# Optimization experiments

Hardware: AMD Instinct MI355X
Metric: run time of the kernel (lower is better)

## Reference

```python
import jax, jax.numpy as jnp
import numpy as np

C = 512
GROUPS = 8
EPS = 1e-5


def setup_inputs() -> dict:
    key = jax.random.key(0)
    ks = jax.random.split(key, 7)
    B, H, W = 16, 32, 32
    x = jax.random.normal(ks[0], (B, C, H, W), dtype=jnp.float32)
    gamma = jnp.ones((C,), jnp.float32)
    beta = jnp.zeros((C,), jnp.float32)
    # 1x1 convs stored as [out, in] matrices
    w_qkv = jax.random.normal(ks[1], (3 * C, C), dtype=jnp.float32) * (1.0 / np.sqrt(C))
    b_qkv = jax.random.normal(ks[2], (3 * C,), dtype=jnp.float32) * 0.02
    w_proj = jax.random.normal(ks[3], (C, C), dtype=jnp.float32) * (1.0 / np.sqrt(C))
    b_proj = jax.random.normal(ks[4], (C,), dtype=jnp.float32) * 0.02
    return {"x": x, "gamma": gamma, "beta": beta, "w_qkv": w_qkv,
            "b_qkv": b_qkv, "w_proj": w_proj, "b_proj": b_proj}


def _group_norm(x, gamma, beta):
    B, Cc, H, W = x.shape
    xg = x.reshape(B, GROUPS, Cc // GROUPS, H, W)
    mean = xg.mean(axis=(2, 3, 4), keepdims=True)
    var = xg.var(axis=(2, 3, 4), keepdims=True)
    xg = (xg - mean) * jax.lax.rsqrt(var + EPS)
    x = xg.reshape(B, Cc, H, W)
    return x * gamma[None, :, None, None] + beta[None, :, None, None]


def reference(x, gamma, beta, w_qkv, b_qkv, w_proj, b_proj):
    B, Cc, H, W = x.shape
    N = H * W
    h = _group_norm(x, gamma, beta)  # [B,C,H,W]
    hf = h.reshape(B, Cc, N)  # [B,C,N]
    # 1x1 conv == matmul over channel dim
    qkv = jnp.einsum('oc,bcn->bon', w_qkv, hf) + b_qkv[None, :, None]  # [B,3C,N]
    q, k, v = jnp.split(qkv, 3, axis=1)  # each [B,C,N]
    scale = 1.0 / jnp.sqrt(jnp.float32(Cc))
    # attn[b,i,j] = sum_c q[b,c,i] * k[b,c,j]
    attn = jnp.einsum('bci,bcj->bij', q, k) * scale  # [B,N,N]
    attn = jax.nn.softmax(attn, axis=-1)
    out = jnp.einsum('bij,bcj->bci', attn, v)  # [B,C,N]
    out = jnp.einsum('oc,bcn->bon', w_proj, out) + b_proj[None, :, None]
    return x + out.reshape(B, Cc, H, W)
```

## Files before the change

### kernel.cpp

```cpp
#include <hip/hip_runtime.h>
#include <hip/hip_bf16.h>

typedef unsigned short u16;
typedef unsigned int u32;
typedef __attribute__((ext_vector_type(8))) short short8;
typedef __attribute__((ext_vector_type(4))) float floatx4;

#define BATCH 16
#define CDIM 512
#define NSPAT 1024
#define NGROUP 8

__device__ __forceinline__ u16 f2bf(float f) {
    unsigned u = __float_as_uint(f);
    u += 0x7FFFu + ((u >> 16) & 1u);
    return (u16)(u >> 16);
}
__device__ __forceinline__ u32 f2bf2(float lo, float hi) {
    __hip_bfloat162 h = __float22bfloat162_rn(make_float2(lo, hi));
    return *(u32*)&h;
}

__device__ __forceinline__ void load_lds16(const void* g, void* l) {
    __builtin_amdgcn_global_load_lds(
        (const __attribute__((address_space(1))) unsigned int*)g,
        (__attribute__((address_space(3))) unsigned int*)l, 16, 0, 0);
}

#define SBAR0 __builtin_amdgcn_sched_barrier(0)
#define BARRIER { SBAR0; __builtin_amdgcn_s_barrier(); SBAR0; }

__global__ __launch_bounds__(256) void prep_kernel(
    const float* __restrict__ w_qkv, const float* __restrict__ w_proj,
    const float* __restrict__ b_qkv, const float* __restrict__ x,
    u16* __restrict__ wmega, u16* __restrict__ wproj_bf, u16* __restrict__ wv_t,
    float* __restrict__ stats, float* __restrict__ lsums, float* __restrict__ bpv) {
    int b = blockIdx.x;
    int tid = threadIdx.x;
    if (b < 768) {
        const float* src = (b < 512) ? w_qkv : w_proj;
        u16* dst = (b < 512) ? wmega : wproj_bf;
        int i = (b < 512 ? b : b - 512) * 256 + tid;
        float4 v = ((const float4*)src)[i];
        u32* d = (u32*)dst;
        d[i * 2] = f2bf2(v.x, v.y);
        d[i * 2 + 1] = f2bf2(v.z, v.w);
        return;
    }
    if (b < 832) {
        __shared__ u16 t[64 * 66];
        int bt = b - 768;
        int tx = bt & 7, ty = bt >> 3;
        const float* src = w_qkv + (size_t)(1024 + ty * 64) * CDIM + tx * 64;
#pragma unroll
        for (int p = 0; p < 4; ++p) {
            int r = p * 16 + (tid >> 4);
            int c4 = (tid & 15) << 2;
            float4 v = *(const float4*)(src + (size_t)r * CDIM + c4);
            u16* d = &t[r * 66 + c4];
            d[0] = f2bf(v.x); d[1] = f2bf(v.y); d[2] = f2bf(v.z); d[3] = f2bf(v.w);
        }
        __syncthreads();
        u16* dst = wv_t + (size_t)(tx * 64) * CDIM + ty * 64;
#pragma unroll
        for (int p = 0; p < 4; ++p) {
            int c = p * 16 + (tid >> 4);
            int r4 = (tid & 15) << 2;
            ushort4 o;
            o.x = t[(r4 + 0) * 66 + c];
            o.y = t[(r4 + 1) * 66 + c];
            o.z = t[(r4 + 2) * 66 + c];
            o.w = t[(r4 + 3) * 66 + c];
            *(ushort4*)(dst + (size_t)c * CDIM + r4) = o;
        }
        return;
    }
    if (b < 960) {
        __shared__ float rs[4], rss[4];
        int bg = b - 832;
        const float4* xv = (const float4*)(x + (size_t)bg * 65536);
        float s = 0.f, ss = 0.f;
        for (int i = tid; i < 16384; i += 256) {
            float4 v = xv[i];
            s += v.x + v.y + v.z + v.w;
            ss += v.x * v.x + v.y * v.y + v.z * v.z + v.w * v.w;
        }
#pragma unroll
        for (int off = 32; off; off >>= 1) { s += __shfl_down(s, off); ss += __shfl_down(ss, off); }
        int wave = tid >> 6, lane = tid & 63;
        if (lane == 0) { rs[wave] = s; rss[wave] = ss; }
        __syncthreads();
        if (tid == 0) {
            float S1 = rs[0] + rs[1] + rs[2] + rs[3];
            float S2 = rss[0] + rss[1] + rss[2] + rss[3];
            float mean = S1 * (1.f / 65536.f);
            float var = S2 * (1.f / 65536.f) - mean * mean;
            stats[bg * 2] = mean;
            stats[bg * 2 + 1] = rsqrtf(var + 1e-5f);
        }
        return;
    }
    if (b < 976) {
        ((float4*)lsums)[(b - 960) * 256 + tid] = (float4){0.f, 0.f, 0.f, 0.f};
        return;
    }
    {
        int o0 = (b - 976) * 64;
        int wave = tid >> 6, lane = tid & 63;
        const float4* bvv = (const float4*)(b_qkv + 1024);
        float4 v0 = bvv[lane * 2], v1 = bvv[lane * 2 + 1];
        for (int it = 0; it < 16; ++it) {
            int o = o0 + wave * 16 + it;
            const float4* wr = (const float4*)(w_proj + (size_t)o * CDIM);
            float4 a0 = wr[lane * 2], a1 = wr[lane * 2 + 1];
            float s = a0.x * v0.x + a0.y * v0.y + a0.z * v0.z + a0.w * v0.w
                    + a1.x * v1.x + a1.y * v1.y + a1.z * v1.z + a1.w * v1.w;
#pragma unroll
            for (int off = 32; off; off >>= 1) s += __shfl_down(s, off);
            if (lane == 0) bpv[o] = s;
        }
    }
}

__device__ __forceinline__ void stage_tile(
    const u16* __restrict__ Ab, const u16* __restrict__ Bb, int lda, int ldb,
    int m0, int n0, int k0, u16* As, u16* Bs) {
    int tid = threadIdx.x;
#pragma unroll
    for (int it = 0; it < 4; ++it) {
        int c = it * 256 + tid;
        int r = c >> 3, p = c & 7;
        int kc = p ^ (r & 7);
        load_lds16(Ab + (size_t)(m0 + r) * lda + k0 + (kc << 3), &As[c << 3]);
        load_lds16(Bb + (size_t)(n0 + r) * ldb + k0 + (kc << 3), &Bs[c << 3]);
    }
}

__device__ __forceinline__ void compute_tile(
    const u16* As, const u16* Bs, int wm, int wn, int quad, int lrow,
    floatx4 (&acc)[4][4]) {
#pragma unroll
    for (int s = 0; s < 2; ++s) {
        short8 af[4], bf[4];
#pragma unroll
        for (int i = 0; i < 4; ++i) {
            int R = wm + i * 16 + lrow;
            int p = (s * 4 + quad) ^ (R & 7);
            af[i] = *(const short8*)&As[(R << 6) + (p << 3)];
        }
#pragma unroll
        for (int j = 0; j < 4; ++j) {
            int R = wn + j * 16 + lrow;
            int p = (s * 4 + quad) ^ (R & 7);
            bf[j] = *(const short8*)&Bs[(R << 6) + (p << 3)];
        }
#pragma unroll
        for (int i = 0; i < 4; ++i)
#pragma unroll
            for (int j = 0; j < 4; ++j)
                acc[i][j] = __builtin_amdgcn_mfma_f32_16x16x32_bf16(af[i], bf[j], acc[i][j], 0, 0, 0);
    }
}

__device__ __forceinline__ void gemm_core_sb(
    const u16* __restrict__ Ab, const u16* __restrict__ Bb, int K, int lda, int ldb,
    int m0, int n0, u16* As, u16* Bs, floatx4 (&acc)[4][4]) {
    int tid = threadIdx.x;
    int lane = tid & 63, wave = tid >> 6, quad = lane >> 4, lrow = lane & 15;
    int wm = (wave >> 1) << 6, wn = (wave & 1) << 6;
    for (int k0 = 0; k0 < K; k0 += 64) {
        stage_tile(Ab, Bb, lda, ldb, m0, n0, k0, As, Bs);
        __syncthreads();
        compute_tile(As, Bs, wm, wn, quad, lrow, acc);
        __syncthreads();
    }
}

#define ACC_INIT floatx4 acc[4][4]; \
    _Pragma("unroll") for (int i = 0; i < 4; ++i) \
    _Pragma("unroll") for (int j = 0; j < 4; ++j) acc[i][j] = (floatx4){0.f, 0.f, 0.f, 0.f};

#define EPILOG_IDX int lane = threadIdx.x & 63, wave = threadIdx.x >> 6; \
    int quad = lane >> 4, lrow = lane & 15; \
    int wm = (wave >> 1) << 6, wn = (wave & 1) << 6;

__device__ __forceinline__ void issueA2(
    const u16* __restrict__ Ab, int lda, int m0, int t, int h, u16* smem) {
    int tid = threadIdx.x;
    u16* base = smem + (t & 1) * 16384 + h * 8192;
#pragma unroll
    for (int l = 0; l < 2; ++l) {
        int c = l * 512 + tid;
        int rho = c >> 3, p = c & 7;
        int kc = p ^ (rho & 7);
        int r = ((rho >> 6) << 7) | (h << 6) | (rho & 63);
        load_lds16(Ab + (size_t)(m0 + r) * lda + (t << 6) + (kc << 3), base + (c << 3));
    }
}
__device__ __forceinline__ void issueB2(
    const u16* __restrict__ Bb, int ldb, int n0, int t, int h, u16* smem) {
    int tid = threadIdx.x;
    u16* base = smem + 32768 + (t & 1) * 16384 + h * 8192;
#pragma unroll
    for (int l = 0; l < 2; ++l) {
        int c = l * 512 + tid;
        int rho = c >> 3, p = c & 7;
        int kc = p ^ (rho & 7);
        int r = ((rho >> 5) << 6) | (h << 5) | (rho & 31);
        load_lds16(Bb + (size_t)(n0 + r) * ldb + (t << 6) + (kc << 3), base + (c << 3));
    }
}

template <bool RD_AF, int QM, int QN>
__device__ __forceinline__ void comp2(
    const u16* smem, int slot, int wrow, int wcol, int quad, int lrow,
    short8 (&af)[8], floatx4 (&acc)[8][4]) {
    const u16* Ah = smem + slot * 16384 + QM * 8192;
    const u16* Bh = smem + 32768 + slot * 16384 + QN * 8192;
    short8 bf[4];
#pragma unroll
    for (int ks = 0; ks < 2; ++ks) {
        if (RD_AF) {
#pragma unroll
            for (int i = 0; i < 4; ++i) {
                int rho = wrow * 64 + i * 16 + lrow;
                int p = (ks * 4 + quad) ^ (lrow & 7);
                af[ks * 4 + i] = *(const short8*)&Ah[(rho << 6) + (p << 3)];
            }
        }
#pragma unroll
        for (int j = 0; j < 2; ++j) {
            int rho = wcol * 32 + j * 16 + lrow;
            int p = (ks * 4 + quad) ^ (lrow & 7);
            bf[ks * 2 + j] = *(const short8*)&Bh[(rho << 6) + (p << 3)];
        }
    }
    asm volatile("s_waitcnt lgkmcnt(0)" ::: "memory");
    SBAR0;
    __builtin_amdgcn_s_setprio(1);
#pragma unroll
    for (int ks = 0; ks < 2; ++ks)
#pragma unroll
        for (int i = 0; i < 4; ++i)
#pragma unroll
            for (int j = 0; j < 2; ++j)
                acc[QM * 4 + i][QN * 2 + j] = __builtin_amdgcn_mfma_f32_16x16x32_bf16(
                    af[ks * 4 + i], bf[ks * 2 + j], acc[QM * 4 + i][QN * 2 + j], 0, 0, 0);
    __builtin_amdgcn_s_setprio(0);
}

__device__ __forceinline__ void gemm256x256(
    const u16* __restrict__ Ab, const u16* __restrict__ Bb, int K, int lda, int ldb,
    int m0, int n0, u16* smem, floatx4 (&acc)[8][4]) {
    int tid = threadIdx.x;
    int lane = tid & 63, wave = tid >> 6;
    int quad = lane >> 4, lrow = lane & 15;
    int wrow = wave >> 2, wcol = wave & 3;
    int nt = K >> 6;
    short8 af[8];
    issueA2(Ab, lda, m0, 0, 0, smem);
    issueB2(Bb, ldb, n0, 0, 0, smem);
    issueB2(Bb, ldb, n0, 0, 1, smem);
    issueA2(Ab, lda, m0, 0, 1, smem);
    for (int t = 0; t < nt; ++t) {
        int slot = t & 1;
        bool nxt = (t + 1 < nt);
        asm volatile("s_waitcnt vmcnt(4)" ::: "memory");
        BARRIER;
        if (nxt) issueA2(Ab, lda, m0, t + 1, 0, smem);
        comp2<true, 0, 0>(smem, slot, wrow, wcol, quad, lrow, af, acc);
        BARRIER;
        if (nxt) { asm volatile("s_waitcnt vmcnt(4)" ::: "memory"); }
        else     { asm volatile("s_waitcnt vmcnt(2)" ::: "memory"); }
        BARRIER;
        if (nxt) issueB2(Bb, ldb, n0, t + 1, 0, smem);
        comp2<false, 0, 1>(smem, slot, wrow, wcol, quad, lrow, af, acc);
        BARRIER;
        if (nxt) { asm volatile("s_waitcnt vmcnt(4)" ::: "memory"); }
        else     { asm volatile("s_waitcnt vmcnt(0)" ::: "memory"); }
        BARRIER;
        if (nxt) issueB2(Bb, ldb, n0, t + 1, 1, smem);
        comp2<true, 1, 0>(smem, slot, wrow, wcol, quad, lrow, af, acc);
        BARRIER;
        if (nxt) issueA2(Ab, lda, m0, t + 1, 1, smem);
        comp2<false, 1, 1>(smem, slot, wrow, wcol, quad, lrow, af, acc);
        BARRIER;
    }
}

__device__ __forceinline__ void issueA4(
    const u16* __restrict__ Ab, int lda, int m0, int t, u16* smem) {
    int tid = threadIdx.x;
    u16* base = smem + (t & 1) * 16384;
#pragma unroll
    for (int l = 0; l < 4; ++l) {
        int c = l * 512 + tid;
        int rho = c >> 3, p = c & 7;
        int kc = p ^ (rho & 7);
        load_lds16(Ab + (size_t)(m0 + rho) * lda + (t << 6) + (kc << 3), base + (c << 3));
    }
}
__device__ __forceinline__ void issueB4(
    const u16* __restrict__ Bb, int ldb, int n0, int t, int h, u16* smem) {
    int tid = threadIdx.x;
    u16* base = smem + 32768 + (t & 1) * 8192 + h * 4096;
    int rho = tid >> 3, p = tid & 7;
    int kc = p ^ (rho & 7);
    int r = ((rho >> 5) << 6) | (h << 5) | (rho & 31);
    load_lds16(Bb + (size_t)(n0 + r) * ldb + (t << 6) + (kc << 3), base + (tid << 3));
}

template <bool RD_AF, int QN>
__device__ __forceinline__ void comp4(
    const u16* smem, int slot, int wrow, int wcol, int quad, int lrow,
    short8 (&af)[8], floatx4 (&acc)[4][4]) {
    const u16* Ah = smem + slot * 16384;
    const u16* Bh = smem + 32768 + slot * 8192 + QN * 4096;
    short8 bf[4];
#pragma unroll
    for (int ks = 0; ks < 2; ++ks) {
        if (RD_AF) {
#pragma unroll
            for (int i = 0; i < 4; ++i) {
                int rho = wrow * 64 + i * 16 + lrow;
                int p = (ks * 4 + quad) ^ (lrow & 7);
                af[ks * 4 + i] = *(const short8*)&Ah[(rho << 6) + (p << 3)];
            }
        }
#pragma unroll
        for (int j = 0; j < 2; ++j) {
            int rho = wcol * 32 + j * 16 + lrow;
            int p = (ks * 4 + quad) ^ (lrow & 7);
            bf[ks * 2 + j] = *(const short8*)&Bh[(rho << 6) + (p << 3)];
        }
    }
    asm volatile("s_waitcnt lgkmcnt(0)" ::: "memory");
    SBAR0;
    __builtin_amdgcn_s_setprio(1);
#pragma unroll
    for (int ks = 0; ks < 2; ++ks)
#pragma unroll
        for (int i = 0; i < 4; ++i)
#pragma unroll
            for (int j = 0; j < 2; ++j)
                acc[i][QN * 2 + j] = __builtin_amdgcn_mfma_f32_16x16x32_bf16(
                    af[ks * 4 + i], bf[ks * 2 + j], acc[i][QN * 2 + j], 0, 0, 0);
    __builtin_amdgcn_s_setprio(0);
}

__device__ __forceinline__ void gemm256x128(
    const u16* __restrict__ Ab, const u16* __restrict__ Bb, int K, int lda, int ldb,
    int m0, int n0, u16* smem, floatx4 (&acc)[4][4]) {
    int tid = threadIdx.x;
    int lane = tid & 63, wave = tid >> 6;
    int quad = lane >> 4, lrow = lane & 15;
    int wrow = wave >> 1, wcol = wave & 1;
    int nt = K >> 6;
    short8 af[8];
    issueB4(Bb, ldb, n0, 0, 0, smem);
    issueA4(Ab, lda, m0, 0, smem);
    issueB4(Bb, ldb, n0, 0, 1, smem);
    for (int t = 0; t < nt; ++t) {
        int slot = t & 1;
        bool nxt = (t + 1 < nt);
        asm volatile("s_waitcnt vmcnt(1)" ::: "memory");
        BARRIER;
        if (nxt) { issueB4(Bb, ldb, n0, t + 1, 0, smem); issueA4(Ab, lda, m0, t + 1, smem); }
        comp4<true, 0>(smem, slot, wrow, wcol, quad, lrow, af, acc);
        BARRIER;
        if (nxt) { asm volatile("s_waitcnt vmcnt(5)" ::: "memory"); }
        else     { asm volatile("s_waitcnt vmcnt(0)" ::: "memory"); }
        BARRIER;
        if (nxt) issueB4(Bb, ldb, n0, t + 1, 1, smem);
        comp4<false, 1>(smem, slot, wrow, wcol, quad, lrow, af, acc);
        BARRIER;
    }
}

#define ACC_INIT84 floatx4 acc[8][4]; \
    _Pragma("unroll") for (int i = 0; i < 8; ++i) \
    _Pragma("unroll") for (int j = 0; j < 4; ++j) acc[i][j] = (floatx4){0.f, 0.f, 0.f, 0.f};

#define ACC_INIT44 floatx4 acc[4][4]; \
    _Pragma("unroll") for (int i = 0; i < 4; ++i) \
    _Pragma("unroll") for (int j = 0; j < 4; ++j) acc[i][j] = (floatx4){0.f, 0.f, 0.f, 0.f};

#define TSTR 66
__global__ __launch_bounds__(256) void gn_wpv_kernel(
    const float* __restrict__ x, const float* __restrict__ gamma, const float* __restrict__ beta,
    const float* __restrict__ stats, u16* __restrict__ hT,
    const u16* __restrict__ wproj_bf, const u16* __restrict__ wv_t, u16* __restrict__ wmega) {
    __shared__ u16 smem[2 * 128 * 64];
    int tid = threadIdx.x;
    if (blockIdx.z == 16) {
        if (blockIdx.x >= 4 || blockIdx.y >= 4) return;
        int m0 = blockIdx.y << 7, n0 = blockIdx.x << 7;
        ACC_INIT;
        gemm_core_sb(wproj_bf, wv_t, CDIM, CDIM, CDIM, m0, n0, smem, smem + 128 * 64, acc);
        EPILOG_IDX;
#pragma unroll
        for (int i = 0; i < 4; ++i)
#pragma unroll
            for (int j = 0; j < 4; ++j)
#pragma unroll
                for (int r = 0; r < 4; ++r) {
                    int R = m0 + wm + i * 16 + (quad << 2) + r;
                    int Cc = n0 + wn + j * 16 + lrow;
                    wmega[(size_t)(1024 + R) * CDIM + Cc] = f2bf(acc[i][j][r]);
                }
        return;
    }
    u16* t = smem;
    int b = blockIdx.z, c0 = blockIdx.y << 6, n0 = blockIdx.x << 6;
    const float* xb = x + ((size_t)b * CDIM + c0) * NSPAT + n0;
#pragma unroll
    for (int p = 0; p < 4; ++p) {
        int cl = p * 16 + (tid >> 4);
        int nl = (tid & 15) << 2;
        int c = c0 + cl;
        int bg = b * NGROUP + (c >> 6);
        float ga = gamma[c] * stats[bg * 2 + 1];
        float be = beta[c] - stats[bg * 2] * ga;
        float4 v = *(const float4*)(xb + (size_t)cl * NSPAT + nl);
        u16* dst = &t[cl * TSTR + nl];
        dst[0] = f2bf(v.x * ga + be);
        dst[1] = f2bf(v.y * ga + be);
        dst[2] = f2bf(v.z * ga + be);
        dst[3] = f2bf(v.w * ga + be);
    }
    __syncthreads();
    u16* hb = hT + ((size_t)b * NSPAT + n0) * CDIM + c0;
#pragma unroll
    for (int p = 0; p < 4; ++p) {
        int nl = p * 16 + (tid >> 4);
        int cl4 = (tid & 15) << 2;
        ushort4 o;
        o.x = t[(cl4 + 0) * TSTR + nl];
        o.y = t[(cl4 + 1) * TSTR + nl];
        o.z = t[(cl4 + 2) * TSTR + nl];
        o.w = t[(cl4 + 3) * TSTR + nl];
        *(ushort4*)(hb + (size_t)nl * CDIM + cl4) = o;
    }
}

__global__ __launch_bounds__(512, 2) void qkv_kernel(
    const u16* __restrict__ wmega, const u16* __restrict__ hT,
    const float* __restrict__ b_qkv, const float* __restrict__ bpv,
    u16* __restrict__ qkT, u16* __restrict__ WV) {
    extern __shared__ u16 smem[];
    int z = blockIdx.x;
    int n0 = blockIdx.y << 8;
    int m0 = blockIdx.z << 8;
    const u16* Bb = hT + (size_t)z * CDIM * NSPAT;
    ACC_INIT84;
    gemm256x256(wmega, Bb, CDIM, CDIM, CDIM, m0, n0, smem, acc);
    int lane = threadIdx.x & 63, wave = threadIdx.x >> 6;
    int quad = lane >> 4, lrow = lane & 15;
    int wrow = wave >> 2, wcol = wave & 3;
    if (blockIdx.z < 4) {
        u16* qk = qkT + (size_t)z * NSPAT * NSPAT;
#pragma unroll
        for (int mf = 0; mf < 8; ++mf) {
            int R0 = m0 + wrow * 128 + mf * 16 + (quad << 2);
            float4 bv = *(const float4*)&b_qkv[R0];
#pragma unroll
            for (int nf = 0; nf < 4; ++nf) {
                int Cc = n0 + wcol * 64 + nf * 16 + lrow;
                uint2 u;
                u.x = f2bf2(acc[mf][nf][0] + bv.x, acc[mf][nf][1] + bv.y);
                u.y = f2bf2(acc[mf][nf][2] + bv.z, acc[mf][nf][3] + bv.w);
                *(uint2*)&qk[(size_t)Cc * NSPAT + R0] = u;
            }
        }
    } else {
        u16* Wp = WV + (size_t)z * CDIM * NSPAT;
#pragma unroll
        for (int mf = 0; mf < 8; ++mf) {
            int R = m0 - 1024 + wrow * 128 + mf * 16 + (quad << 2);
            float4 pv = *(const float4*)&bpv[R];
#pragma unroll
            for (int nf = 0; nf < 4; ++nf) {
                int Cc = n0 + wcol * 64 + nf * 16 + lrow;
                Wp[(size_t)(R + 0) * NSPAT + Cc] = f2bf(acc[mf][nf][0] + pv.x);
                Wp[(size_t)(R + 1) * NSPAT + Cc] = f2bf(acc[mf][nf][1] + pv.y);
                Wp[(size_t)(R + 2) * NSPAT + Cc] = f2bf(acc[mf][nf][2] + pv.z);
                Wp[(size_t)(R + 3) * NSPAT + Cc] = f2bf(acc[mf][nf][3] + pv.w);
            }
        }
    }
}

__global__ __launch_bounds__(512, 2) void scores_kernel(
    const u16* __restrict__ qkT, u16* __restrict__ P, float* __restrict__ lsums, float scale) {
    extern __shared__ u16 smem[];
    int z = blockIdx.x;
    int n0 = blockIdx.y << 8;
    int m0 = blockIdx.z << 8;
    const u16* qb = qkT + (size_t)z * NSPAT * NSPAT;
    ACC_INIT84;
    gemm256x256(qb + CDIM, qb, CDIM, NSPAT, NSPAT, m0, n0, smem, acc);
    int lane = threadIdx.x & 63, wave = threadIdx.x >> 6;
    int quad = lane >> 4, lrow = lane & 15;
    int wrow = wave >> 2, wcol = wave & 3;
    u16* Pp = P + (size_t)z * NSPAT * NSPAT;
    float* ls = lsums + (size_t)z * NSPAT;
#pragma unroll
    for (int nf = 0; nf < 4; ++nf) {
        int Ci = n0 + wcol * 64 + nf * 16 + lrow;
        float part = 0.f;
#pragma unroll
        for (int mf = 0; mf < 8; ++mf) {
            int Rj0 = m0 + wrow * 128 + mf * 16 + (quad << 2);
            float e0 = __expf(acc[mf][nf][0] * scale);
            float e1 = __expf(acc[mf][nf][1] * scale);
            float e2 = __expf(acc[mf][nf][2] * scale);
            float e3 = __expf(acc[mf][nf][3] * scale);
            part += (e0 + e1) + (e2 + e3);
            uint2 u;
            u.x = f2bf2(e0, e1);
            u.y = f2bf2(e2, e3);
            *(uint2*)&Pp[(size_t)Ci * NSPAT + Rj0] = u;
        }
        part += __shfl_xor(part, 16);
        part += __shfl_xor(part, 32);
        if (lane < 16) atomicAdd(&ls[Ci], part);
    }
}

__global__ __launch_bounds__(512, 2) void final_kernel(
    const u16* __restrict__ WV, const u16* __restrict__ P, const float* __restrict__ lsums,
    const float* __restrict__ bias, const float* __restrict__ x, float* __restrict__ out) {
    extern __shared__ u16 smem[];
    int z = blockIdx.x;
    int n0 = blockIdx.y << 7;
    int m0 = blockIdx.z << 8;
    const u16* Pb = P + (size_t)z * NSPAT * NSPAT;
    const u16* WVb = WV + (size_t)z * CDIM * NSPAT;
    ACC_INIT44;
    gemm256x128(Pb, WVb, NSPAT, NSPAT, NSPAT, m0, n0, smem, acc);
    int lane = threadIdx.x & 63, wave = threadIdx.x >> 6;
    int quad = lane >> 4, lrow = lane & 15;
    int wrow = wave >> 1, wcol = wave & 1;
    float* Op = out + (size_t)z * CDIM * NSPAT;
    const float* xr = x + (size_t)z * CDIM * NSPAT;
    const float* li = lsums + (size_t)z * NSPAT;
#pragma unroll
    for (int mf = 0; mf < 4; ++mf) {
        int Ri0 = m0 + wrow * 64 + mf * 16 + (quad << 2);
        float4 lv = *(const float4*)&li[Ri0];
        float s0 = __builtin_amdgcn_rcpf(lv.x);
        float s1 = __builtin_amdgcn_rcpf(lv.y);
        float s2 = __builtin_amdgcn_rcpf(lv.z);
        float s3 = __builtin_amdgcn_rcpf(lv.w);
#pragma unroll
        for (int nf = 0; nf < 4; ++nf) {
            int Co = n0 + wcol * 64 + nf * 16 + lrow;
            float bv = bias[Co];
            size_t off = (size_t)Co * NSPAT + Ri0;
            float4 xv = *(const float4*)&xr[off];
            float4 o;
            o.x = acc[mf][nf][0] * s0 + bv + xv.x;
            o.y = acc[mf][nf][1] * s1 + bv + xv.y;
            o.z = acc[mf][nf][2] * s2 + bv + xv.z;
            o.w = acc[mf][nf][3] * s3 + bv + xv.w;
            *(float4*)&Op[off] = o;
        }
    }
}

extern "C" void kernel_launch(void* const* d_in, const int* in_sizes, int n_in,
                              void* d_out, int out_size, void* d_ws, size_t ws_size,
                              hipStream_t stream) {
    const float* x      = (const float*)d_in[0];
    const float* gamma  = (const float*)d_in[1];
    const float* beta   = (const float*)d_in[2];
    const float* w_qkv  = (const float*)d_in[3];
    const float* b_qkv  = (const float*)d_in[4];
    const float* w_proj = (const float*)d_in[5];
    const float* b_proj = (const float*)d_in[6];
    float* out = (float*)d_out;

    const size_t CN = (size_t)CDIM * NSPAT;
    const size_t NN = (size_t)NSPAT * NSPAT;
    const float SCALE = 0.044194173824159216f;
    const int LDS_BIG = 131072;
    const int LDS_MED = 98304;

    static bool lds_attr_done = false;
    if (!lds_attr_done) {
        hipFuncSetAttribute((const void*)qkv_kernel,
                            hipFuncAttributeMaxDynamicSharedMemorySize, LDS_BIG);
        hipFuncSetAttribute((const void*)scores_kernel,
                            hipFuncAttributeMaxDynamicSharedMemorySize, LDS_BIG);
        hipFuncSetAttribute((const void*)final_kernel,
                            hipFuncAttributeMaxDynamicSharedMemorySize, LDS_MED);
        lds_attr_done = true;
    }

    char* ws = (char*)d_ws;
    float* stats   = (float*)ws;
    float* bpv     = (float*)(ws + 1024);
    u16* wmega     = (u16*)(ws + 4096);
    u16* wproj_bf  = wmega + (size_t)3 * CDIM * CDIM;
    u16* wv_t      = wproj_bf + (size_t)CDIM * CDIM;
    u16* hT        = wv_t + (size_t)CDIM * CDIM;
    u16* qkT       = hT + BATCH * CN;
    u16* WV        = qkT + BATCH * NN;
    u16* P         = WV + BATCH * CN;
    float* lsums   = (float*)(P + BATCH * NN);

    prep_kernel<<<984, 256, 0, stream>>>(
        w_qkv, w_proj, b_qkv, x, wmega, wproj_bf, wv_t, stats, lsums, bpv);

    gn_wpv_kernel<<<dim3(16, 8, 17), 256, 0, stream>>>(
        x, gamma, beta, stats, hT, wproj_bf, wv_t, wmega);

    qkv_kernel<<<dim3(BATCH, 4, 6), 512, LDS_BIG, stream>>>(
        wmega, hT, b_qkv, bpv, qkT, WV);

    scores_kernel<<<dim3(BATCH, 4, 4), 512, LDS_BIG, stream>>>(qkT, P, lsums, SCALE);

    final_kernel<<<dim3(BATCH, 4, 4), 512, LDS_MED, stream>>>(WV, P, lsums, b_proj, x, out);
}
```

Measured before the change: 138.7 us.

## Simplify GEMM mainloops to whole-tile prefetch with one wait per K-step

Replaces the fine-grained quarter-tile ping-pong schedules in the 256x256 and 256x128 GEMM loops. The old loops issued loads for the next tile piece by piece, with barriers and setprio around each sub-compute. The new loops prefetch the whole next K-tile at the start of each iteration, wait until the current tile has landed, then run all MFMAs in one block. This removes many barriers and waitcnts, but loads are no longer interleaved with compute at sub-tile granularity. Register pressure also rises because all B fragments are held at once.

```diff
diff --git a/kernel.cpp b/kernel.cpp
--- a/kernel.cpp
+++ b/kernel.cpp
@@ -211,169 +211,146 @@
     }
 }
 
-template <bool RD_AF, int QM, int QN>
-__device__ __forceinline__ void comp2(
-    const u16* smem, int slot, int wrow, int wcol, int quad, int lrow,
-    short8 (&af)[8], floatx4 (&acc)[8][4]) {
-    const u16* Ah = smem + slot * 16384 + QM * 8192;
-    const u16* Bh = smem + 32768 + slot * 16384 + QN * 8192;
-    short8 bf[4];
-#pragma unroll
-    for (int ks = 0; ks < 2; ++ks) {
-        if (RD_AF) {
+__device__ __forceinline__ void gemm256x256(
+    const u16* __restrict__ Ab, const u16* __restrict__ Bb, int K, int lda, int ldb,
+    int m0, int n0, u16* smem, floatx4 (&acc)[8][4]) {
+    int tid = threadIdx.x;
+    int lane = tid & 63, wave = tid >> 6;
+    int quad = lane >> 4, lrow = lane & 15;
+    int wrow = wave >> 2, wcol = wave & 3;
+    int nt = K >> 6;
+    issueA2(Ab, lda, m0, 0, 0, smem);
+    issueA2(Ab, lda, m0, 0, 1, smem);
+    issueB2(Bb, ldb, n0, 0, 0, smem);
+    issueB2(Bb, ldb, n0, 0, 1, smem);
+    for (int t = 0; t < nt; ++t) {
+        int slot = t & 1;
+        BARRIER;
+        if (t + 1 < nt) {
+            issueA2(Ab, lda, m0, t + 1, 0, smem);
+            issueA2(Ab, lda, m0, t + 1, 1, smem);
+            issueB2(Bb, ldb, n0, t + 1, 0, smem);
+            issueB2(Bb, ldb, n0, t + 1, 1, smem);
+            asm volatile("s_waitcnt vmcnt(8)" ::: "memory");
+        } else {
+            asm volatile("s_waitcnt vmcnt(0)" ::: "memory");
+        }
+        BARRIER;
+        const u16* Ah = smem + slot * 16384;
+        const u16* Bh = smem + 32768 + slot * 16384;
+        short8 bf[2][4];
+#pragma unroll
+        for (int qn = 0; qn < 2; ++qn)
+#pragma unroll
+            for (int ks = 0; ks < 2; ++ks)
+#pragma unroll
+                for (int j = 0; j < 2; ++j) {
+                    int rho = wcol * 32 + j * 16 + lrow;
+                    int p = (ks * 4 + quad) ^ (lrow & 7);
+                    bf[qn][ks * 2 + j] = *(const short8*)&Bh[qn * 8192 + (rho << 6) + (p << 3)];
+                }
+#pragma unroll
+        for (int qm = 0; qm < 2; ++qm) {
+            short8 af[8];
+#pragma unroll
+            for (int ks = 0; ks < 2; ++ks)
+#pragma unroll
+                for (int i = 0; i < 4; ++i) {
+                    int rho = wrow * 64 + i * 16 + lrow;
+                    int p = (ks * 4 + quad) ^ (lrow & 7);
+                    af[ks * 4 + i] = *(const short8*)&Ah[qm * 8192 + (rho << 6) + (p << 3)];
+                }
+#pragma unroll
+            for (int ks = 0; ks < 2; ++ks)
+#pragma unroll
+                for (int i = 0; i < 4; ++i)
+#pragma unroll
+                    for (int qn = 0; qn < 2; ++qn)
+#pragma unroll
+                        for (int j = 0; j < 2; ++j)
+                            acc[qm * 4 + i][qn * 2 + j] = __builtin_amdgcn_mfma_f32_16x16x32_bf16(
+                                af[ks * 4 + i], bf[qn][ks * 2 + j], acc[qm * 4 + i][qn * 2 + j], 0, 0, 0);
+        }
+    }
+}
+
+__device__ __forceinline__ void issueA4(
+    const u16* __restrict__ Ab, int lda, int m0, int t, u16* smem) {
+    int tid = threadIdx.x;
+    u16* base = smem + (t & 1) * 16384;
+#pragma unroll
+    for (int l = 0; l < 4; ++l) {
+        int c = l * 512 + tid;
+        int rho = c >> 3, p = c & 7;
+        int kc = p ^ (rho & 7);
+        load_lds16(Ab + (size_t)(m0 + rho) * lda + (t << 6) + (kc << 3), base + (c << 3));
+    }
+}
+__device__ __forceinline__ void issueB4(
+    const u16* __restrict__ Bb, int ldb, int n0, int t, int h, u16* smem) {
+    int tid = threadIdx.x;
+    u16* base = smem + 32768 + (t & 1) * 8192 + h * 4096;
+    int rho = tid >> 3, p = tid & 7;
+    int kc = p ^ (rho & 7);
+    int r = ((rho >> 5) << 6) | (h << 5) | (rho & 31);
+    load_lds16(Bb + (size_t)(n0 + r) * ldb + (t << 6) + (kc << 3), base + (tid << 3));
+}
+
+__device__ __forceinline__ void gemm256x128(
+    const u16* __restrict__ Ab, const u16* __restrict__ Bb, int K, int lda, int ldb,
+    int m0, int n0, u16* smem, floatx4 (&acc)[4][4]) {
+    int tid = threadIdx.x;
+    int lane = tid & 63, wave = tid >> 6;
+    int quad = lane >> 4, lrow = lane & 15;
+    int wrow = wave >> 1, wcol = wave & 1;
+    int nt = K >> 6;
+    issueA4(Ab, lda, m0, 0, smem);
+    issueB4(Bb, ldb, n0, 0, 0, smem);
+    issueB4(Bb, ldb, n0, 0, 1, smem);
+    for (int t = 0; t < nt; ++t) {
+        int slot = t & 1;
+        BARRIER;
+        if (t + 1 < nt) {
+            issueA4(Ab, lda, m0, t + 1, smem);
+            issueB4(Bb, ldb, n0, t + 1, 0, smem);
+            issueB4(Bb, ldb, n0, t + 1, 1, smem);
+            asm volatile("s_waitcnt vmcnt(6)" ::: "memory");
+        } else {
+            asm volatile("s_waitcnt vmcnt(0)" ::: "memory");
+        }
+        BARRIER;
+        const u16* Ah = smem + slot * 16384;
+        const u16* Bh = smem + 32768 + slot * 8192;
+        short8 bf[2][4];
+#pragma unroll
+        for (int qn = 0; qn < 2; ++qn)
+#pragma unroll
+            for (int ks = 0; ks < 2; ++ks)
+#pragma unroll
+                for (int j = 0; j < 2; ++j) {
+                    int rho = wcol * 32 + j * 16 + lrow;
+                    int p = (ks * 4 + quad) ^ (lrow & 7);
+                    bf[qn][ks * 2 + j] = *(const short8*)&Bh[qn * 4096 + (rho << 6) + (p << 3)];
+                }
+        short8 af[8];
+#pragma unroll
+        for (int ks = 0; ks < 2; ++ks)
 #pragma unroll
             for (int i = 0; i < 4; ++i) {
                 int rho = wrow * 64 + i * 16 + lrow;
                 int p = (ks * 4 + quad) ^ (lrow & 7);
                 af[ks * 4 + i] = *(const short8*)&Ah[(rho << 6) + (p << 3)];
             }
-        }
-#pragma unroll
-        for (int j = 0; j < 2; ++j) {
-            int rho = wcol * 32 + j * 16 + lrow;
-            int p = (ks * 4 + quad) ^ (lrow & 7);
-            bf[ks * 2 + j] = *(const short8*)&Bh[(rho << 6) + (p << 3)];
-        }
-    }
-    asm volatile("s_waitcnt lgkmcnt(0)" ::: "memory");
-    SBAR0;
-    __builtin_amdgcn_s_setprio(1);
-#pragma unroll
-    for (int ks = 0; ks < 2; ++ks)
-#pragma unroll
-        for (int i = 0; i < 4; ++i)
-#pragma unroll
-            for (int j = 0; j < 2; ++j)
-                acc[QM * 4 + i][QN * 2 + j] = __builtin_amdgcn_mfma_f32_16x16x32_bf16(
-                    af[ks * 4 + i], bf[ks * 2 + j], acc[QM * 4 + i][QN * 2 + j], 0, 0, 0);
-    __builtin_amdgcn_s_setprio(0);
-}
-
-__device__ __forceinline__ void gemm256x256(
-    const u16* __restrict__ Ab, const u16* __restrict__ Bb, int K, int lda, int ldb,
-    int m0, int n0, u16* smem, floatx4 (&acc)[8][4]) {
-    int tid = threadIdx.x;
-    int lane = tid & 63, wave = tid >> 6;
-    int quad = lane >> 4, lrow = lane & 15;
-    int wrow = wave >> 2, wcol = wave & 3;
-    int nt = K >> 6;
-    short8 af[8];
-    issueA2(Ab, lda, m0, 0, 0, smem);
-    issueB2(Bb, ldb, n0, 0, 0, smem);
-    issueB2(Bb, ldb, n0, 0, 1, smem);
-    issueA2(Ab, lda, m0, 0, 1, smem);
-    for (int t = 0; t < nt; ++t) {
-        int slot = t & 1;
-        bool nxt = (t + 1 < nt);
-        asm volatile("s_waitcnt vmcnt(4)" ::: "memory");
-        BARRIER;
-        if (nxt) issueA2(Ab, lda, m0, t + 1, 0, smem);
-        comp2<true, 0, 0>(smem, slot, wrow, wcol, quad, lrow, af, acc);
-        BARRIER;
-        if (nxt) { asm volatile("s_waitcnt vmcnt(4)" ::: "memory"); }
-        else     { asm volatile("s_waitcnt vmcnt(2)" ::: "memory"); }
-        BARRIER;
-        if (nxt) issueB2(Bb, ldb, n0, t + 1, 0, smem);
-        comp2<false, 0, 1>(smem, slot, wrow, wcol, quad, lrow, af, acc);
-        BARRIER;
-        if (nxt) { asm volatile("s_waitcnt vmcnt(4)" ::: "memory"); }
-        else     { asm volatile("s_waitcnt vmcnt(0)" ::: "memory"); }
-        BARRIER;
-        if (nxt) issueB2(Bb, ldb, n0, t + 1, 1, smem);
-        comp2<true, 1, 0>(smem, slot, wrow, wcol, quad, lrow, af, acc);
-        BARRIER;
-        if (nxt) issueA2(Ab, lda, m0, t + 1, 1, smem);
-        comp2<false, 1, 1>(smem, slot, wrow, wcol, quad, lrow, af, acc);
-        BARRIER;
-    }
-}
-
-__device__ __forceinline__ void issueA4(
-    const u16* __restrict__ Ab, int lda, int m0, int t, u16* smem) {
-    int tid = threadIdx.x;
-    u16* base = smem + (t & 1) * 16384;
-#pragma unroll
-    for (int l = 0; l < 4; ++l) {
-        int c = l * 512 + tid;
-        int rho = c >> 3, p = c & 7;
-        int kc = p ^ (rho & 7);
-        load_lds16(Ab + (size_t)(m0 + rho) * lda + (t << 6) + (kc << 3), base + (c << 3));
-    }
-}
-__device__ __forceinline__ void issueB4(
-    const u16* __restrict__ Bb, int ldb, int n0, int t, int h, u16* smem) {
-    int tid = threadIdx.x;
-    u16* base = smem + 32768 + (t & 1) * 8192 + h * 4096;
-    int rho = tid >> 3, p = tid & 7;
-    int kc = p ^ (rho & 7);
-    int r = ((rho >> 5) << 6) | (h << 5) | (rho & 31);
-    load_lds16(Bb + (size_t)(n0 + r) * ldb + (t << 6) + (kc << 3), base + (tid << 3));
-}
-
-template <bool RD_AF, int QN>
-__device__ __forceinline__ void comp4(
-    const u16* smem, int slot, int wrow, int wcol, int quad, int lrow,
-    short8 (&af)[8], floatx4 (&acc)[4][4]) {
-    const u16* Ah = smem + slot * 16384;
-    const u16* Bh = smem + 32768 + slot * 8192 + QN * 4096;
-    short8 bf[4];
-#pragma unroll
-    for (int ks = 0; ks < 2; ++ks) {
-        if (RD_AF) {
-#pragma unroll
-            for (int i = 0; i < 4; ++i) {
-                int rho = wrow * 64 + i * 16 + lrow;
-                int p = (ks * 4 + quad) ^ (lrow & 7);
-                af[ks * 4 + i] = *(const short8*)&Ah[(rho << 6) + (p << 3)];
-            }
-        }
-#pragma unroll
-        for (int j = 0; j < 2; ++j) {
-            int rho = wcol * 32 + j * 16 + lrow;
-            int p = (ks * 4 + quad) ^ (lrow & 7);
-            bf[ks * 2 + j] = *(const short8*)&Bh[(rho << 6) + (p << 3)];
-        }
-    }
-    asm volatile("s_waitcnt lgkmcnt(0)" ::: "memory");
-    SBAR0;
-    __builtin_amdgcn_s_setprio(1);
-#pragma unroll
-    for (int ks = 0; ks < 2; ++ks)
-#pragma unroll
-        for (int i = 0; i < 4; ++i)
-#pragma unroll
-            for (int j = 0; j < 2; ++j)
-                acc[i][QN * 2 + j] = __builtin_amdgcn_mfma_f32_16x16x32_bf16(
-                    af[ks * 4 + i], bf[ks * 2 + j], acc[i][QN * 2 + j], 0, 0, 0);
-    __builtin_amdgcn_s_setprio(0);
-}
-
-__device__ __forceinline__ void gemm256x128(
-    const u16* __restrict__ Ab, const u16* __restrict__ Bb, int K, int lda, int ldb,
-    int m0, int n0, u16* smem, floatx4 (&acc)[4][4]) {
-    int tid = threadIdx.x;
-    int lane = tid & 63, wave = tid >> 6;
-    int quad = lane >> 4, lrow = lane & 15;
-    int wrow = wave >> 1, wcol = wave & 1;
-    int nt = K >> 6;
-    short8 af[8];
-    issueB4(Bb, ldb, n0, 0, 0, smem);
-    issueA4(Ab, lda, m0, 0, smem);
-    issueB4(Bb, ldb, n0, 0, 1, smem);
-    for (int t = 0; t < nt; ++t) {
-        int slot = t & 1;
-        bool nxt = (t + 1 < nt);
-        asm volatile("s_waitcnt vmcnt(1)" ::: "memory");
-        BARRIER;
-        if (nxt) { issueB4(Bb, ldb, n0, t + 1, 0, smem); issueA4(Ab, lda, m0, t + 1, smem); }
-        comp4<true, 0>(smem, slot, wrow, wcol, quad, lrow, af, acc);
-        BARRIER;
-        if (nxt) { asm volatile("s_waitcnt vmcnt(5)" ::: "memory"); }
-        else     { asm volatile("s_waitcnt vmcnt(0)" ::: "memory"); }
-        BARRIER;
-        if (nxt) issueB4(Bb, ldb, n0, t + 1, 1, smem);
-        comp4<false, 1>(smem, slot, wrow, wcol, quad, lrow, af, acc);
-        BARRIER;
+#pragma unroll
+        for (int ks = 0; ks < 2; ++ks)
+#pragma unroll
+            for (int i = 0; i < 4; ++i)
+#pragma unroll
+                for (int qn = 0; qn < 2; ++qn)
+#pragma unroll
+                    for (int j = 0; j < 2; ++j)
+                        acc[i][qn * 2 + j] = __builtin_amdgcn_mfma_f32_16x16x32_bf16(
+                            af[ks * 4 + i], bf[qn][ks * 2 + j], acc[i][qn * 2 + j], 0, 0, 0);
     }
 }
 
```

Result: faster. 134.8 us (-2.8%).
